# Kernel tuning notes

Hardware: AMD Instinct MI355X
Metric: run time of the kernel (lower is better)

The kernel has to match this reference:

```python
import jax, jax.numpy as jnp
import numpy as np
from jax import lax
from jax.scipy.special import logsumexp

INSIZE = 256
NBASE = 4
SIZE = 2 * NBASE * (NBASE + 1)  # 40


def setup_inputs() -> dict:
    key = jax.random.key(0)
    kx, kw, kb = jax.random.split(key, 3)
    x = jax.random.normal(kx, (2048, 256, INSIZE), dtype=jnp.float32)
    W = jax.random.normal(kw, (SIZE, INSIZE), dtype=jnp.float32) / np.sqrt(INSIZE)
    b = 0.5 * jax.random.normal(kb, (SIZE,), dtype=jnp.float32)
    return {"x": x, "W": W, "b": b}


def global_norm_flipflop(scores):
    # scores: (T, N, C) with C = 2*nbase*(nbase+1)
    T, N, C = scores.shape
    nbase = int(np.sqrt(C / 2))
    assert 2 * nbase * (nbase + 1) == C

    fwd0 = jnp.zeros((N, 2 * nbase), dtype=scores.dtype)
    logZ0 = logsumexp(fwd0, axis=1, keepdims=True)  # (N, 1) = log(2*nbase)
    fwd0 = fwd0 - logZ0

    def step(carry, sc_t):
        fwd, logZ = carry
        # (N, nbase+1, 2*nbase): transition scores into each destination row
        sc = fwd[:, None, :] + sc_t.reshape(N, nbase + 1, 2 * nbase)
        base1 = logsumexp(sc[:, :nbase], axis=2)  # flip states (N, nbase)
        base2 = jnp.logaddexp(sc[:, nbase, :nbase], sc[:, nbase, nbase:])  # flop (N, nbase)
        new_state = jnp.concatenate([base1, base2], axis=1)  # (N, 2*nbase)
        factors = logsumexp(new_state, axis=1, keepdims=True)
        return (new_state - factors, logZ + factors), None

    (_, logZ), _ = lax.scan(step, (fwd0, logZ0), scores)
    return scores - logZ / T  # broadcast (N,1) over (T,N,C)


def reference(x, W, b):
    y = 5.0 * jnp.tanh(x @ W.T + b)  # (T, N, 40)
    return global_norm_flipflop(y)
```

## Files before the change

kernel.cpp:

```cpp
#include <hip/hip_runtime.h>

#define T_DIM 2048
#define N_DIM 256
#define K_DIM 256
#define C_DIM 40
#define CHUNK 32
#define NCHUNK 64
#define NTILES (T_DIM * N_DIM / 16)

#define LOG2E_F 1.44269504088896340736f
#define LN2_F   0.69314718055994530942f
#define NEGBIG  (-1.0e30f)

typedef short bf16x8 __attribute__((ext_vector_type(8)));
typedef float f32x4  __attribute__((ext_vector_type(4)));
typedef unsigned int u32x4 __attribute__((ext_vector_type(4)));

__device__ __forceinline__ float fexp2(float x) { return exp2f(x); }
__device__ __forceinline__ float flog2(float x) { return log2f(x); }
__device__ __forceinline__ float frcp(float x) { return __frcp_rn(x); }

__device__ __forceinline__ unsigned int pkbf(float lo, float hi)
{
    unsigned int a = __float_as_uint(lo);
    unsigned int b = __float_as_uint(hi);
    a += 0x7fffu + ((a >> 16) & 1u);
    b += 0x7fffu + ((b >> 16) & 1u);
    return (a >> 16) | (b & 0xffff0000u);
}

__device__ __forceinline__ bf16x8 pack8(float4 lo, float4 hi)
{
    u32x4 t;
    t[0] = pkbf(lo.x, lo.y);
    t[1] = pkbf(lo.z, lo.w);
    t[2] = pkbf(hi.x, hi.y);
    t[3] = pkbf(hi.z, hi.w);
    return __builtin_bit_cast(bf16x8, t);
}

__device__ __forceinline__ float tanh5(float v)
{
    const float e = fexp2(fabsf(v) * (2.0f * LOG2E_F));
    const float t = 1.0f - 2.0f * frcp(e + 1.0f);
    return 5.0f * copysignf(t, v);
}

__global__ __launch_bounds__(256, 3) void k1_gemm_tanh(
    const float* __restrict__ x, const float* __restrict__ W,
    const float* __restrict__ b, float* __restrict__ y)
{
    const int tid  = threadIdx.x;
    const int wave = tid >> 6;
    const int lane = tid & 63;
    const int lr   = lane & 15;
    const int kg   = lane >> 4;

    bf16x8 wf[3][8];
    float  bv[3];
#pragma unroll
    for (int nt = 0; nt < 3; ++nt) {
        const int c = nt * 16 + lr;
        const bool valid = (c < C_DIM);
        const float* __restrict__ wp =
            W + (size_t)(valid ? c : 0) * K_DIM + kg * 8;
        bv[nt] = valid ? b[c] : 0.0f;
#pragma unroll
        for (int ks = 0; ks < 8; ++ks) {
            float4 lo = *(const float4*)(wp + ks * 32);
            float4 hi = *(const float4*)(wp + ks * 32 + 4);
            if (!valid) { lo = make_float4(0, 0, 0, 0); hi = lo; }
            wf[nt][ks] = pack8(lo, hi);
        }
    }

    const int wid    = blockIdx.x * 4 + wave;
    const int nwaves = gridDim.x * 4;

    for (int tile = wid; tile < NTILES; tile += nwaves) {
        const float* __restrict__ xp =
            x + ((size_t)tile * 16 + lr) * K_DIM + kg * 8;

        f32x4 af[3];
#pragma unroll
        for (int nt = 0; nt < 3; ++nt) {
            af[nt][0] = bv[nt]; af[nt][1] = bv[nt];
            af[nt][2] = bv[nt]; af[nt][3] = bv[nt];
        }

#pragma unroll
        for (int ks = 0; ks < 8; ++ks) {
            const float4 lo = *(const float4*)(xp + ks * 32);
            const float4 hi = *(const float4*)(xp + ks * 32 + 4);
            const bf16x8 a = pack8(lo, hi);
            af[0] = __builtin_amdgcn_mfma_f32_16x16x32_bf16(a, wf[0][ks], af[0], 0, 0, 0);
            af[1] = __builtin_amdgcn_mfma_f32_16x16x32_bf16(a, wf[1][ks], af[1], 0, 0, 0);
            af[2] = __builtin_amdgcn_mfma_f32_16x16x32_bf16(a, wf[2][ks], af[2], 0, 0, 0);
        }

        float* __restrict__ yrow =
            y + ((size_t)tile * 16 + kg * 4) * C_DIM;
#pragma unroll
        for (int nt = 0; nt < 3; ++nt) {
            const int col = nt * 16 + lr;
            if (col < C_DIM) {
#pragma unroll
                for (int r = 0; r < 4; ++r)
                    yrow[r * C_DIM + col] = tanh5(af[nt][r]);
            }
        }
    }
}

__global__ __launch_bounds__(256) void k2_chunks(
    const float* __restrict__ y, float* __restrict__ cmat)
{
    const int tid  = threadIdx.x;
    const int wave = tid >> 6;
    const int lane = tid & 63;
    const int task = lane >> 3;
    const int c    = lane & 7;
    const int g    = blockIdx.x & (NCHUNK - 1);
    const int n    = ((blockIdx.x >> 6) << 5) + (wave << 3) + task;

    float col[8];
#pragma unroll
    for (int j = 0; j < 8; ++j) col[j] = (j == c) ? 0.0f : NEGBIG;

    const float* __restrict__ yp =
        y + ((size_t)(g * CHUNK) * N_DIM + (size_t)n) * C_DIM;

#pragma unroll 1
    for (int s = 0; s < CHUNK; ++s) {
        float sc[C_DIM];
        const float4* p4 = (const float4*)yp;
#pragma unroll
        for (int q = 0; q < 10; ++q) {
            const float4 v = p4[q];
            sc[4 * q + 0] = v.x * LOG2E_F;
            sc[4 * q + 1] = v.y * LOG2E_F;
            sc[4 * q + 2] = v.z * LOG2E_F;
            sc[4 * q + 3] = v.w * LOG2E_F;
        }
        float nc[8];
#pragma unroll
        for (int d = 0; d < 4; ++d) {
            float tv[8];
#pragma unroll
            for (int j = 0; j < 8; ++j) tv[j] = sc[d * 8 + j] + col[j];
            float m = tv[0];
#pragma unroll
            for (int j = 1; j < 8; ++j) m = fmaxf(m, tv[j]);
            float ss = 0.0f;
#pragma unroll
            for (int j = 0; j < 8; ++j) ss += fexp2(tv[j] - m);
            nc[d] = m + flog2(ss);
        }
#pragma unroll
        for (int i = 0; i < 4; ++i) {
            const float a  = sc[32 + i] + col[i];
            const float bb = sc[36 + i] + col[i + 4];
            const float m  = fmaxf(a, bb);
            const float ss = fexp2(a - m) + fexp2(bb - m);
            nc[4 + i] = m + flog2(ss);
        }
#pragma unroll
        for (int j = 0; j < 8; ++j) col[j] = nc[j];
        yp += (size_t)N_DIM * C_DIM;
    }
    float* __restrict__ op = cmat + (((size_t)g * 8 + c) * N_DIM + n) * 8;
#pragma unroll
    for (int j = 0; j < 8; ++j) op[j] = col[j];
}

__global__ __launch_bounds__(256) void k3_combine(
    const float* __restrict__ cmat, float* __restrict__ corr)
{
    const int tid = threadIdx.x;
    const int d   = tid & 7;
    const int n   = blockIdx.x * 32 + (tid >> 3);

    float v[8];
#pragma unroll
    for (int j = 0; j < 8; ++j) v[j] = 0.0f;

#pragma unroll 1
    for (int g = 0; g < NCHUNK; ++g) {
        const float* mg = cmat + ((size_t)g * 8 * N_DIM + n) * 8 + d;
        float mm[8];
#pragma unroll
        for (int j = 0; j < 8; ++j) mm[j] = mg[(size_t)j * N_DIM * 8];
        float tv[8];
#pragma unroll
        for (int j = 0; j < 8; ++j) tv[j] = mm[j] + v[j];
        float m = tv[0];
#pragma unroll
        for (int j = 1; j < 8; ++j) m = fmaxf(m, tv[j]);
        float ss = 0.0f;
#pragma unroll
        for (int j = 0; j < 8; ++j) ss += fexp2(tv[j] - m);
        const float nv = m + flog2(ss);
#pragma unroll
        for (int j = 0; j < 8; ++j) v[j] = __shfl(nv, j, 8);
    }
    float m = v[0];
#pragma unroll
    for (int j = 1; j < 8; ++j) m = fmaxf(m, v[j]);
    float ss = 0.0f;
#pragma unroll
    for (int j = 0; j < 8; ++j) ss += fexp2(v[j] - m);
    const float lz2 = m + flog2(ss);
    if (d == 0) corr[n] = lz2 * LN2_F / (float)T_DIM;
}

__global__ __launch_bounds__(256) void k4_final(
    float* __restrict__ out, const float* __restrict__ corr)
{
    const unsigned int i = blockIdx.x * 256u + threadIdx.x;
    float4* o4 = (float4*)out;
    float4 v = o4[i];
    const unsigned int n = (i / 10u) & (N_DIM - 1);
    const float cr = corr[n];
    v.x -= cr; v.y -= cr; v.z -= cr; v.w -= cr;
    o4[i] = v;
}

extern "C" void kernel_launch(void* const* d_in, const int* in_sizes, int n_in,
                              void* d_out, int out_size, void* d_ws, size_t ws_size,
                              hipStream_t stream)
{
    const float* x = (const float*)d_in[0];
    const float* W = (const float*)d_in[1];
    const float* b = (const float*)d_in[2];
    float* y = (float*)d_out;

    float* cmat = (float*)d_ws;
    float* corr = (float*)d_ws + (size_t)NCHUNK * 8 * N_DIM * 8;

    hipLaunchKernelGGL(k1_gemm_tanh, dim3(1024), dim3(256), 0, stream, x, W, b, y);
    hipLaunchKernelGGL(k2_chunks,    dim3(512),  dim3(256), 0, stream, y, cmat);
    hipLaunchKernelGGL(k3_combine,   dim3(8),    dim3(256), 0, stream, cmat, corr);
    hipLaunchKernelGGL(k4_final,     dim3((T_DIM * N_DIM * C_DIM / 4) / 256),
                       dim3(256), 0, stream, y, corr);
}
```

Baseline: 301.2 us.

## Stage bf16 W fragments in LDS and raise GEMM occupancy

Moves the packed bf16 weight fragments and bias out of per-thread registers into shared memory, loaded once per block, and reads them from LDS inside the MFMA loop. This frees about 96 VGPRs so launch bounds can ask for 4 blocks per CU, aiming at more memory-level parallelism on the streaming x loads. It also uses the HIP bf16 conversion intrinsic instead of manual rounding and hardcodes the tile stride. The cost is extra LDS reads per k-step and a grid-size assumption baked into the stride.

```diff
diff --git a/kernel.cpp b/kernel.cpp
--- a/kernel.cpp
+++ b/kernel.cpp
@@ -1,4 +1,5 @@
 #include <hip/hip_runtime.h>
+#include <hip/hip_bf16.h>
 
 #define T_DIM 2048
 #define N_DIM 256
@@ -14,29 +15,34 @@
 
 typedef short bf16x8 __attribute__((ext_vector_type(8)));
 typedef float f32x4  __attribute__((ext_vector_type(4)));
-typedef unsigned int u32x4 __attribute__((ext_vector_type(4)));
 
 __device__ __forceinline__ float fexp2(float x) { return exp2f(x); }
 __device__ __forceinline__ float flog2(float x) { return log2f(x); }
 __device__ __forceinline__ float frcp(float x) { return __frcp_rn(x); }
 
-__device__ __forceinline__ unsigned int pkbf(float lo, float hi)
-{
-    unsigned int a = __float_as_uint(lo);
-    unsigned int b = __float_as_uint(hi);
-    a += 0x7fffu + ((a >> 16) & 1u);
-    b += 0x7fffu + ((b >> 16) & 1u);
-    return (a >> 16) | (b & 0xffff0000u);
-}
-
-__device__ __forceinline__ bf16x8 pack8(float4 lo, float4 hi)
-{
-    u32x4 t;
-    t[0] = pkbf(lo.x, lo.y);
-    t[1] = pkbf(lo.z, lo.w);
-    t[2] = pkbf(hi.x, hi.y);
-    t[3] = pkbf(hi.z, hi.w);
-    return __builtin_bit_cast(bf16x8, t);
+__device__ __forceinline__ unsigned int pk2(float a, float b)
+{
+    __hip_bfloat162 h = __float22bfloat162_rn(make_float2(a, b));
+    unsigned int r;
+    __builtin_memcpy(&r, &h, sizeof(r));
+    return r;
+}
+
+__device__ __forceinline__ uint4 pack8u(float4 lo, float4 hi)
+{
+    uint4 t;
+    t.x = pk2(lo.x, lo.y);
+    t.y = pk2(lo.z, lo.w);
+    t.z = pk2(hi.x, hi.y);
+    t.w = pk2(hi.z, hi.w);
+    return t;
+}
+
+__device__ __forceinline__ bf16x8 as_bf16x8(uint4 u)
+{
+    bf16x8 r;
+    __builtin_memcpy(&r, &u, sizeof(r));
+    return r;
 }
 
 __device__ __forceinline__ float tanh5(float v)
@@ -46,68 +52,74 @@
     return 5.0f * copysignf(t, v);
 }
 
-__global__ __launch_bounds__(256, 3) void k1_gemm_tanh(
+__global__ __launch_bounds__(256, 4) void k1_gemm_tanh(
     const float* __restrict__ x, const float* __restrict__ W,
     const float* __restrict__ b, float* __restrict__ y)
 {
-    const int tid  = threadIdx.x;
+    __shared__ __align__(16) uint4 wlds[24 * 64];
+    __shared__ float blds[48];
+
+    const int tid = threadIdx.x;
+
+#pragma unroll
+    for (int p = 0; p < 6; ++p) {
+        const int f    = p * 256 + tid;
+        const int l    = f & 63;
+        const int frag = f >> 6;
+        const int nt   = frag % 3;
+        const int ks   = frag / 3;
+        const int col  = nt * 16 + (l & 15);
+        const int kb   = ks * 32 + (l >> 4) * 8;
+        float4 lo = make_float4(0, 0, 0, 0), hi = lo;
+        if (col < C_DIM) {
+            lo = *(const float4*)(W + (size_t)col * K_DIM + kb);
+            hi = *(const float4*)(W + (size_t)col * K_DIM + kb + 4);
+        }
+        wlds[frag * 64 + l] = pack8u(lo, hi);
+    }
+    if (tid < 48) blds[tid] = (tid < C_DIM) ? b[tid] : 0.0f;
+    __syncthreads();
+
     const int wave = tid >> 6;
     const int lane = tid & 63;
     const int lr   = lane & 15;
     const int kg   = lane >> 4;
 
-    bf16x8 wf[3][8];
-    float  bv[3];
-#pragma unroll
-    for (int nt = 0; nt < 3; ++nt) {
-        const int c = nt * 16 + lr;
-        const bool valid = (c < C_DIM);
-        const float* __restrict__ wp =
-            W + (size_t)(valid ? c : 0) * K_DIM + kg * 8;
-        bv[nt] = valid ? b[c] : 0.0f;
-#pragma unroll
-        for (int ks = 0; ks < 8; ++ks) {
-            float4 lo = *(const float4*)(wp + ks * 32);
-            float4 hi = *(const float4*)(wp + ks * 32 + 4);
-            if (!valid) { lo = make_float4(0, 0, 0, 0); hi = lo; }
-            wf[nt][ks] = pack8(lo, hi);
-        }
-    }
-
-    const int wid    = blockIdx.x * 4 + wave;
-    const int nwaves = gridDim.x * 4;
-
-    for (int tile = wid; tile < NTILES; tile += nwaves) {
+    const float bc0 = blds[lr];
+    const float bc1 = blds[16 + lr];
+    const float bc2 = blds[32 + lr];
+
+    const int wid = blockIdx.x * 4 + wave;
+
+#pragma unroll 1
+    for (int tile = wid; tile < NTILES; tile += 4096) {
         const float* __restrict__ xp =
             x + ((size_t)tile * 16 + lr) * K_DIM + kg * 8;
 
-        f32x4 af[3];
-#pragma unroll
-        for (int nt = 0; nt < 3; ++nt) {
-            af[nt][0] = bv[nt]; af[nt][1] = bv[nt];
-            af[nt][2] = bv[nt]; af[nt][3] = bv[nt];
-        }
+        f32x4 af0 = {bc0, bc0, bc0, bc0};
+        f32x4 af1 = {bc1, bc1, bc1, bc1};
+        f32x4 af2 = {bc2, bc2, bc2, bc2};
 
 #pragma unroll
         for (int ks = 0; ks < 8; ++ks) {
             const float4 lo = *(const float4*)(xp + ks * 32);
             const float4 hi = *(const float4*)(xp + ks * 32 + 4);
-            const bf16x8 a = pack8(lo, hi);
-            af[0] = __builtin_amdgcn_mfma_f32_16x16x32_bf16(a, wf[0][ks], af[0], 0, 0, 0);
-            af[1] = __builtin_amdgcn_mfma_f32_16x16x32_bf16(a, wf[1][ks], af[1], 0, 0, 0);
-            af[2] = __builtin_amdgcn_mfma_f32_16x16x32_bf16(a, wf[2][ks], af[2], 0, 0, 0);
-        }
-
-        float* __restrict__ yrow =
-            y + ((size_t)tile * 16 + kg * 4) * C_DIM;
-#pragma unroll
-        for (int nt = 0; nt < 3; ++nt) {
-            const int col = nt * 16 + lr;
-            if (col < C_DIM) {
-#pragma unroll
-                for (int r = 0; r < 4; ++r)
-                    yrow[r * C_DIM + col] = tanh5(af[nt][r]);
-            }
+            const bf16x8 a = as_bf16x8(pack8u(lo, hi));
+            const bf16x8 w0 = *(const bf16x8*)&wlds[(ks * 3 + 0) * 64 + lane];
+            const bf16x8 w1 = *(const bf16x8*)&wlds[(ks * 3 + 1) * 64 + lane];
+            const bf16x8 w2 = *(const bf16x8*)&wlds[(ks * 3 + 2) * 64 + lane];
+            af0 = __builtin_amdgcn_mfma_f32_16x16x32_bf16(a, w0, af0, 0, 0, 0);
+            af1 = __builtin_amdgcn_mfma_f32_16x16x32_bf16(a, w1, af1, 0, 0, 0);
+            af2 = __builtin_amdgcn_mfma_f32_16x16x32_bf16(a, w2, af2, 0, 0, 0);
+        }
+
+        float* __restrict__ yrow = y + ((size_t)tile * 16 + kg * 4) * C_DIM;
+#pragma unroll
+        for (int r = 0; r < 4; ++r) {
+            yrow[r * C_DIM + lr]      = tanh5(af0[r]);
+            yrow[r * C_DIM + 16 + lr] = tanh5(af1[r]);
+            if (lr < 8)
+                yrow[r * C_DIM + 32 + lr] = tanh5(af2[r]);
         }
     }
 }
```

Result: faster. 262.1 us (-13.0%).
